# Optimization experiments

Measured on AMD Instinct MI355X. Metric: run time of the kernel, lower is better.

Reference implementation:

```python
import jax, jax.numpy as jnp
import numpy as np

REFRACTORY_PERIOD = 5
DAMPENING_FACTOR = 0.3


def setup_inputs() -> dict:
    key = jax.random.key(0)
    B, T, N = 32, 4096, 256
    x = jax.random.normal(key, (B, T, N), dtype=jnp.float32)
    return {"x": x}


def _refractory_scan(x):
    # x: [B, T, N]; scan over time keeping refractory counter q resident.
    B, T, N = x.shape
    xt = jnp.swapaxes(x, 0, 1)  # [T, B, N]

    def step(q, x_t):
        cond = (x_t > 0) & (q == 0)
        z_t = jnp.where(cond, jnp.ones_like(q), jnp.zeros_like(q))
        q = jnp.maximum(jnp.zeros_like(q), q - 1) + REFRACTORY_PERIOD * z_t
        return q, z_t

    q0 = jnp.zeros((B, N), dtype=x.dtype)
    # Note: the t=0 case in the original (z0 = x0>0, q = R*z0) is exactly the
    # first step of this scan starting from q0 = 0.
    _, z = jax.lax.scan(step, q0, xt)
    return jnp.swapaxes(z, 0, 1)  # [B, T, N]


def reference(x) -> jnp.ndarray:
    # Forward value is exactly z_forward (the surrogate-gradient straight-through
    # construction leaves the value unchanged).
    return _refractory_scan(x)
```

## Files before the change

kernel.cpp:

```cpp
#include <hip/hip_runtime.h>
#include <cstdint>
#include <cstddef>

#define BB 32
#define TT 4096
#define NNV 64
#define CC 16
#define PSUB 16
#define PG 16
#define NCH 256

__global__ __launch_bounds__(1024, 8) void refrac_fused(const float* __restrict__ x,
                                                        float* __restrict__ z,
                                                        uint32_t* __restrict__ msg) {
    const int tid = threadIdx.x;
    const int pg = blockIdx.x >> 5;
    const int b  = blockIdx.x & 31;
    const int psub = tid >> 6;
    const int n4 = tid & 63;
    const int p = pg * PSUB + psub;

    const float4* __restrict__ xv = reinterpret_cast<const float4*>(x)
        + ((size_t)b * TT + (size_t)p * CC) * NNV + n4;

    uint32_t cur[4] = {0u, 0u, 0u, 0u};
    #pragma unroll
    for (int jb = 0; jb < CC; jb += 8) {
        float4 buf[8];
        #pragma unroll
        for (int u = 0; u < 8; ++u)
            buf[u] = xv[(size_t)(jb + u) * NNV];
        #pragma unroll
        for (int u = 0; u < 8; ++u) {
            const int j = jb + u;
            const float fv[4] = {buf[u].x, buf[u].y, buf[u].z, buf[u].w};
            #pragma unroll
            for (int c = 0; c < 4; ++c)
                cur[c] |= (fv[c] > 0.0f) ? (1u << j) : 0u;
        }
    }

    __shared__ uint32_t tbl_lds[PSUB][NCH];
    __shared__ uint8_t  ent_lds[PSUB][NCH];

    #pragma unroll
    for (int c = 0; c < 4; ++c) {
        const uint32_t m = cur[c];
        uint32_t tbl = 0;
        #pragma unroll
        for (int e = 0; e < 6; ++e) {
            int na = e;
            #pragma unroll
            for (int it = 0; it < 3; ++it) {
                const uint32_t r = m >> (na & 31);
                const int t = na + __builtin_ctz(r | 0x10000u);
                na = r ? (t + 6) : na;
            }
            const int q = na > CC ? na - CC : 0;
            tbl |= (uint32_t)q << (4 * e);
        }
        tbl_lds[psub][n4 * 4 + c] = tbl;
    }
    __syncthreads();

    if (tid < NCH) {
        const int n = tid;

        if (pg < PG - 1) {
            uint32_t gtab = 0;
            #pragma unroll
            for (int e0 = 0; e0 < 6; ++e0) {
                int e = e0;
                #pragma unroll
                for (int s = 0; s < PSUB; ++s)
                    e = (int)((tbl_lds[s][n] >> (4 * e)) & 0xFu);
                gtab |= (uint32_t)e << (4 * e0);
            }
            __hip_atomic_store(msg + (((size_t)b * PG + pg) << 8) + n, gtab,
                               __ATOMIC_RELAXED, __HIP_MEMORY_SCOPE_AGENT);
        }

        int e = 0;
        for (int g = 0; g < pg; ++g) {
            const uint32_t* w = msg + (((size_t)b * PG + g) << 8) + n;
            uint32_t wv;
            while ((wv = __hip_atomic_load(w, __ATOMIC_RELAXED,
                                           __HIP_MEMORY_SCOPE_AGENT)) & 0x80000000u)
                __builtin_amdgcn_s_sleep(1);
            e = (int)((wv >> (4 * e)) & 0xFu);
        }

        #pragma unroll
        for (int s = 0; s < PSUB; ++s) {
            ent_lds[s][n] = (uint8_t)e;
            e = (int)((tbl_lds[s][n] >> (4 * e)) & 0xFu);
        }
    }
    __syncthreads();

    float4* __restrict__ zv = reinterpret_cast<float4*>(z)
        + ((size_t)b * TT + (size_t)p * CC) * NNV + n4;

    const uint32_t e4 = reinterpret_cast<const uint32_t*>(ent_lds[psub])[n4];
    uint32_t spk[4];
    #pragma unroll
    for (int c = 0; c < 4; ++c) {
        const uint32_t m = cur[c];
        int na = (int)((e4 >> (8 * c)) & 0xFFu);
        uint32_t s = 0;
        #pragma unroll
        for (int it = 0; it < 3; ++it) {
            const uint32_t r = m >> (na & 31);
            const int t = na + __builtin_ctz(r | 0x10000u);
            s |= r ? (1u << (t & 31)) : 0u;
            na = r ? (t + 6) : na;
        }
        spk[c] = s;
    }

    #pragma unroll
    for (int j = 0; j < CC; ++j) {
        float4 o;
        o.x = ((spk[0] >> j) & 1u) ? 1.0f : 0.0f;
        o.y = ((spk[1] >> j) & 1u) ? 1.0f : 0.0f;
        o.z = ((spk[2] >> j) & 1u) ? 1.0f : 0.0f;
        o.w = ((spk[3] >> j) & 1u) ? 1.0f : 0.0f;
        zv[(size_t)j * NNV] = o;
    }
}

extern "C" void kernel_launch(void* const* d_in, const int* in_sizes, int n_in,
                              void* d_out, int out_size, void* d_ws, size_t ws_size,
                              hipStream_t stream) {
    const float* x = (const float*)d_in[0];
    float* z = (float*)d_out;
    uint32_t* msg = (uint32_t*)d_ws;

    hipMemsetAsync(d_ws, 0xAA, (size_t)BB * PG * NCH * sizeof(uint32_t), stream);

    refrac_fused<<<dim3(BB * PG), 1024, 0, stream>>>(x, z, msg);
}
```

Baseline: 247.5 us.

## Split fused scan into two kernels, replacing cross-block spin-wait with a launch boundary

Replaces the single fused kernel, which spin-waited on atomics to chain per-group transition tables across blocks, with two launches. The first computes per-chunk spike masks and composed transition tables and writes them to workspace. The second loads all prior group tables into LDS, composes them serially, and emits the outputs. Chunk length rises to 32 timesteps with 4 sub-chunks per 256-thread block, which removes the memset and inter-block polling but adds a mask round-trip through global memory and a second launch.

```diff
diff --git a/kernel.cpp b/kernel.cpp
--- a/kernel.cpp
+++ b/kernel.cpp
@@ -5,14 +5,41 @@
 #define BB 32
 #define TT 4096
 #define NNV 64
-#define CC 16
-#define PSUB 16
-#define PG 16
+#define CC 32
+#define PSUB 4
+#define PG 32
 #define NCH 256
 
-__global__ __launch_bounds__(1024, 8) void refrac_fused(const float* __restrict__ x,
-                                                        float* __restrict__ z,
-                                                        uint32_t* __restrict__ msg) {
+__device__ __forceinline__ uint32_t comp6(uint32_t f, uint32_t g) {
+    uint32_t h = 0;
+    #pragma unroll
+    for (int e = 0; e < 6; ++e) {
+        const uint32_t fe = (f >> (4 * e)) & 0xFu;
+        h |= ((g >> (4 * fe)) & 0xFu) << (4 * e);
+    }
+    return h;
+}
+
+__device__ __forceinline__ uint32_t tbl_from_mask(uint32_t m) {
+    uint32_t tbl = 0;
+    #pragma unroll
+    for (int e = 0; e < 6; ++e) {
+        int na = e;
+        #pragma unroll
+        for (int it = 0; it < 6; ++it) {
+            const uint32_t r = (na < 32) ? (m >> na) : 0u;
+            const int t = na + (r ? __builtin_ctz(r) : 0);
+            na = r ? (t + 6) : na;
+        }
+        const int q = na > CC ? na - CC : 0;
+        tbl |= (uint32_t)q << (4 * e);
+    }
+    return tbl;
+}
+
+__global__ __launch_bounds__(256) void k_scan(const float* __restrict__ x,
+                                              uint4* __restrict__ msk,
+                                              uint32_t* __restrict__ gtab) {
     const int tid = threadIdx.x;
     const int pg = blockIdx.x >> 5;
     const int b  = blockIdx.x & 31;
@@ -33,67 +60,59 @@
         #pragma unroll
         for (int u = 0; u < 8; ++u) {
             const int j = jb + u;
-            const float fv[4] = {buf[u].x, buf[u].y, buf[u].z, buf[u].w};
-            #pragma unroll
-            for (int c = 0; c < 4; ++c)
-                cur[c] |= (fv[c] > 0.0f) ? (1u << j) : 0u;
+            cur[0] |= (buf[u].x > 0.0f) ? (1u << j) : 0u;
+            cur[1] |= (buf[u].y > 0.0f) ? (1u << j) : 0u;
+            cur[2] |= (buf[u].z > 0.0f) ? (1u << j) : 0u;
+            cur[3] |= (buf[u].w > 0.0f) ? (1u << j) : 0u;
         }
     }
 
-    __shared__ uint32_t tbl_lds[PSUB][NCH];
-    __shared__ uint8_t  ent_lds[PSUB][NCH];
+    msk[(size_t)blockIdx.x * 256 + tid] = make_uint4(cur[0], cur[1], cur[2], cur[3]);
 
+    __shared__ uint32_t tbl[PSUB][NCH];
+    __shared__ uint32_t aux[2][NCH];
     #pragma unroll
-    for (int c = 0; c < 4; ++c) {
-        const uint32_t m = cur[c];
-        uint32_t tbl = 0;
-        #pragma unroll
-        for (int e = 0; e < 6; ++e) {
-            int na = e;
-            #pragma unroll
-            for (int it = 0; it < 3; ++it) {
-                const uint32_t r = m >> (na & 31);
-                const int t = na + __builtin_ctz(r | 0x10000u);
-                na = r ? (t + 6) : na;
-            }
-            const int q = na > CC ? na - CC : 0;
-            tbl |= (uint32_t)q << (4 * e);
-        }
-        tbl_lds[psub][n4 * 4 + c] = tbl;
-    }
+    for (int c = 0; c < 4; ++c)
+        tbl[psub][n4 * 4 + c] = tbl_from_mask(cur[c]);
+    __syncthreads();
+    aux[0][tid] = comp6(tbl[0][tid], tbl[1][tid]);
+    aux[1][tid] = comp6(tbl[2][tid], tbl[3][tid]);
+    __syncthreads();
+    gtab[(size_t)blockIdx.x * 256 + tid] = comp6(aux[0][tid], aux[1][tid]);
+}
+
+__global__ __launch_bounds__(256) void k_emit(const uint4* __restrict__ msk,
+                                              const uint32_t* __restrict__ gtab,
+                                              float* __restrict__ z) {
+    const int tid = threadIdx.x;
+    const int pg = blockIdx.x >> 5;
+    const int b  = blockIdx.x & 31;
+    const int psub = tid >> 6;
+    const int n4 = tid & 63;
+    const int p = pg * PSUB + psub;
+
+    __shared__ uint32_t gl[PG - 1][NCH];
+    __shared__ uint32_t tbl[PSUB][NCH];
+    __shared__ uint8_t  ent[PSUB][NCH];
+
+    for (int i = tid; i < pg * NCH; i += 256)
+        gl[0][i] = gtab[((size_t)(i >> 8) * 32 + b) * 256 + (i & 255)];
+
+    const uint4 mv = msk[(size_t)blockIdx.x * 256 + tid];
+    uint32_t cur[4] = {mv.x, mv.y, mv.z, mv.w};
+    #pragma unroll
+    for (int c = 0; c < 4; ++c)
+        tbl[psub][n4 * 4 + c] = tbl_from_mask(cur[c]);
     __syncthreads();
 
-    if (tid < NCH) {
-        const int n = tid;
-
-        if (pg < PG - 1) {
-            uint32_t gtab = 0;
-            #pragma unroll
-            for (int e0 = 0; e0 < 6; ++e0) {
-                int e = e0;
-                #pragma unroll
-                for (int s = 0; s < PSUB; ++s)
-                    e = (int)((tbl_lds[s][n] >> (4 * e)) & 0xFu);
-                gtab |= (uint32_t)e << (4 * e0);
-            }
-            __hip_atomic_store(msg + (((size_t)b * PG + pg) << 8) + n, gtab,
-                               __ATOMIC_RELAXED, __HIP_MEMORY_SCOPE_AGENT);
-        }
-
+    {
         int e = 0;
-        for (int g = 0; g < pg; ++g) {
-            const uint32_t* w = msg + (((size_t)b * PG + g) << 8) + n;
-            uint32_t wv;
-            while ((wv = __hip_atomic_load(w, __ATOMIC_RELAXED,
-                                           __HIP_MEMORY_SCOPE_AGENT)) & 0x80000000u)
-                __builtin_amdgcn_s_sleep(1);
-            e = (int)((wv >> (4 * e)) & 0xFu);
-        }
-
+        for (int g = 0; g < pg; ++g)
+            e = (int)((gl[g][tid] >> (4 * e)) & 0xFu);
         #pragma unroll
         for (int s = 0; s < PSUB; ++s) {
-            ent_lds[s][n] = (uint8_t)e;
-            e = (int)((tbl_lds[s][n] >> (4 * e)) & 0xFu);
+            ent[s][tid] = (uint8_t)e;
+            e = (int)((tbl[s][tid] >> (4 * e)) & 0xFu);
         }
     }
     __syncthreads();
@@ -101,7 +120,7 @@
     float4* __restrict__ zv = reinterpret_cast<float4*>(z)
         + ((size_t)b * TT + (size_t)p * CC) * NNV + n4;
 
-    const uint32_t e4 = reinterpret_cast<const uint32_t*>(ent_lds[psub])[n4];
+    const uint32_t e4 = reinterpret_cast<const uint32_t*>(ent[psub])[n4];
     uint32_t spk[4];
     #pragma unroll
     for (int c = 0; c < 4; ++c) {
@@ -109,9 +128,9 @@
         int na = (int)((e4 >> (8 * c)) & 0xFFu);
         uint32_t s = 0;
         #pragma unroll
-        for (int it = 0; it < 3; ++it) {
-            const uint32_t r = m >> (na & 31);
-            const int t = na + __builtin_ctz(r | 0x10000u);
+        for (int it = 0; it < 6; ++it) {
+            const uint32_t r = (na < 32) ? (m >> na) : 0u;
+            const int t = na + (r ? __builtin_ctz(r) : 0);
             s |= r ? (1u << (t & 31)) : 0u;
             na = r ? (t + 6) : na;
         }
@@ -134,9 +153,9 @@
                               hipStream_t stream) {
     const float* x = (const float*)d_in[0];
     float* z = (float*)d_out;
-    uint32_t* msg = (uint32_t*)d_ws;
+    uint4* msk = (uint4*)d_ws;
+    uint32_t* gtab = (uint32_t*)((char*)d_ws + (size_t)BB * PG * PSUB * NCH * 4);
 
-    hipMemsetAsync(d_ws, 0xAA, (size_t)BB * PG * NCH * sizeof(uint32_t), stream);
-
-    refrac_fused<<<dim3(BB * PG), 1024, 0, stream>>>(x, z, msg);
+    k_scan<<<dim3(BB * PG), 256, 0, stream>>>(x, msk, gtab);
+    k_emit<<<dim3(BB * PG), 256, 0, stream>>>(msk, gtab, z);
 }
```

Result: no change. 251.4 us (+1.6%).

## Double chunk length, halve block groups, and chain carry messages sequentially

Applied to the files above, without the earlier changes.

Each thread now handles 32 timesteps instead of 16, so there are half as many block groups per batch, and the spike-finding loops run more iterations to cover the longer mask. Carry propagation across groups changes from each block reading every earlier group's composed table to each block waiting on its immediate predecessor's final state byte. That predecessor only publishes after it has itself waited. This removes the per-block table composition and the multiple global polls, but serializes the decoupled lookback into a strict chain of 8 groups. Each thread also holds more data, and launch bounds drop to 4 blocks per CU.

```diff
diff --git a/kernel.cpp b/kernel.cpp
--- a/kernel.cpp
+++ b/kernel.cpp
@@ -5,14 +5,31 @@
 #define BB 32
 #define TT 4096
 #define NNV 64
-#define CC 16
+#define CC 32
 #define PSUB 16
-#define PG 16
+#define PG 8
 #define NCH 256
 
-__global__ __launch_bounds__(1024, 8) void refrac_fused(const float* __restrict__ x,
+__device__ __forceinline__ uint32_t tbl_from_mask(uint32_t m) {
+    uint32_t tbl = 0;
+    #pragma unroll
+    for (int e = 0; e < 6; ++e) {
+        int na = e;
+        #pragma unroll
+        for (int it = 0; it < 6; ++it) {
+            const uint32_t r = (na < 32) ? (m >> na) : 0u;
+            const int t = na + (r ? __builtin_ctz(r) : 0);
+            na = r ? (t + 6) : na;
+        }
+        const int q = na > CC ? na - CC : 0;
+        tbl |= (uint32_t)q << (4 * e);
+    }
+    return tbl;
+}
+
+__global__ __launch_bounds__(1024, 4) void refrac_fused(const float* __restrict__ x,
                                                         float* __restrict__ z,
-                                                        uint32_t* __restrict__ msg) {
+                                                        uint8_t* __restrict__ msg) {
     const int tid = threadIdx.x;
     const int pg = blockIdx.x >> 5;
     const int b  = blockIdx.x & 31;
@@ -33,10 +50,10 @@
         #pragma unroll
         for (int u = 0; u < 8; ++u) {
             const int j = jb + u;
-            const float fv[4] = {buf[u].x, buf[u].y, buf[u].z, buf[u].w};
-            #pragma unroll
-            for (int c = 0; c < 4; ++c)
-                cur[c] |= (fv[c] > 0.0f) ? (1u << j) : 0u;
+            cur[0] |= (buf[u].x > 0.0f) ? (1u << j) : 0u;
+            cur[1] |= (buf[u].y > 0.0f) ? (1u << j) : 0u;
+            cur[2] |= (buf[u].z > 0.0f) ? (1u << j) : 0u;
+            cur[3] |= (buf[u].w > 0.0f) ? (1u << j) : 0u;
         }
     }
 
@@ -44,64 +61,41 @@
     __shared__ uint8_t  ent_lds[PSUB][NCH];
 
     #pragma unroll
-    for (int c = 0; c < 4; ++c) {
-        const uint32_t m = cur[c];
-        uint32_t tbl = 0;
-        #pragma unroll
-        for (int e = 0; e < 6; ++e) {
-            int na = e;
-            #pragma unroll
-            for (int it = 0; it < 3; ++it) {
-                const uint32_t r = m >> (na & 31);
-                const int t = na + __builtin_ctz(r | 0x10000u);
-                na = r ? (t + 6) : na;
-            }
-            const int q = na > CC ? na - CC : 0;
-            tbl |= (uint32_t)q << (4 * e);
-        }
-        tbl_lds[psub][n4 * 4 + c] = tbl;
-    }
+    for (int c = 0; c < 4; ++c)
+        tbl_lds[psub][n4 * 4 + c] = tbl_from_mask(cur[c]);
     __syncthreads();
 
     if (tid < NCH) {
         const int n = tid;
-
-        if (pg < PG - 1) {
-            uint32_t gtab = 0;
-            #pragma unroll
-            for (int e0 = 0; e0 < 6; ++e0) {
-                int e = e0;
-                #pragma unroll
-                for (int s = 0; s < PSUB; ++s)
-                    e = (int)((tbl_lds[s][n] >> (4 * e)) & 0xFu);
-                gtab |= (uint32_t)e << (4 * e0);
-            }
-            __hip_atomic_store(msg + (((size_t)b * PG + pg) << 8) + n, gtab,
-                               __ATOMIC_RELAXED, __HIP_MEMORY_SCOPE_AGENT);
-        }
+        uint32_t t16[PSUB];
+        #pragma unroll
+        for (int s = 0; s < PSUB; ++s) t16[s] = tbl_lds[s][n];
 
         int e = 0;
-        for (int g = 0; g < pg; ++g) {
-            const uint32_t* w = msg + (((size_t)b * PG + g) << 8) + n;
-            uint32_t wv;
-            while ((wv = __hip_atomic_load(w, __ATOMIC_RELAXED,
-                                           __HIP_MEMORY_SCOPE_AGENT)) & 0x80000000u)
+        if (pg > 0) {
+            const uint8_t* inb = msg + (((size_t)b * PG + (pg - 1)) << 8) + n;
+            uint32_t v;
+            while ((v = __hip_atomic_load(inb, __ATOMIC_RELAXED,
+                                          __HIP_MEMORY_SCOPE_AGENT)) & 0x80u)
                 __builtin_amdgcn_s_sleep(1);
-            e = (int)((wv >> (4 * e)) & 0xFu);
+            e = (int)(v & 0xFu);
         }
-
         #pragma unroll
         for (int s = 0; s < PSUB; ++s) {
             ent_lds[s][n] = (uint8_t)e;
-            e = (int)((tbl_lds[s][n] >> (4 * e)) & 0xFu);
+            e = (int)((t16[s] >> (4 * e)) & 0xFu);
         }
+        if (pg < PG - 1)
+            __hip_atomic_store(msg + (((size_t)b * PG + pg) << 8) + n,
+                               (uint8_t)e, __ATOMIC_RELAXED,
+                               __HIP_MEMORY_SCOPE_AGENT);
     }
     __syncthreads();
 
     float4* __restrict__ zv = reinterpret_cast<float4*>(z)
         + ((size_t)b * TT + (size_t)p * CC) * NNV + n4;
 
-    const uint32_t e4 = reinterpret_cast<const uint32_t*>(ent_lds[psub])[n4];
+    const uint32_t e4 = *reinterpret_cast<const uint32_t*>(&ent_lds[psub][n4 * 4]);
     uint32_t spk[4];
     #pragma unroll
     for (int c = 0; c < 4; ++c) {
@@ -109,9 +103,9 @@
         int na = (int)((e4 >> (8 * c)) & 0xFFu);
         uint32_t s = 0;
         #pragma unroll
-        for (int it = 0; it < 3; ++it) {
-            const uint32_t r = m >> (na & 31);
-            const int t = na + __builtin_ctz(r | 0x10000u);
+        for (int it = 0; it < 6; ++it) {
+            const uint32_t r = (na < 32) ? (m >> na) : 0u;
+            const int t = na + (r ? __builtin_ctz(r) : 0);
             s |= r ? (1u << (t & 31)) : 0u;
             na = r ? (t + 6) : na;
         }
@@ -134,9 +128,9 @@
                               hipStream_t stream) {
     const float* x = (const float*)d_in[0];
     float* z = (float*)d_out;
-    uint32_t* msg = (uint32_t*)d_ws;
+    uint8_t* msg = (uint8_t*)d_ws;
 
-    hipMemsetAsync(d_ws, 0xAA, (size_t)BB * PG * NCH * sizeof(uint32_t), stream);
+    hipMemsetAsync(d_ws, 0xAA, (size_t)BB * PG * NCH, stream);
 
     refrac_fused<<<dim3(BB * PG), 1024, 0, stream>>>(x, z, msg);
 }
```

New measurement: 235.4 us. 1.05x faster.
